# Performance work log

Hardware: AMD Instinct MI355X
Metric: run time of the kernel (lower is better)

Reference implementation:

```python
import jax, jax.numpy as jnp
import numpy as np

B, S, E, H, DH = 256, 256, 384, 6, 64
NEG_INF = -1e9


def setup_inputs() -> dict:
    key = jax.random.key(0)
    ks = jax.random.split(key, 8)
    sc = 0.02
    return {
        "x": jax.random.normal(ks[0], (B, S, E), jnp.float32),
        "Wq": jax.random.normal(ks[1], (H, E, DH), jnp.float32) * sc,
        "Wk": jax.random.normal(ks[2], (H, E, DH), jnp.float32) * sc,
        "Wv": jax.random.normal(ks[3], (H, E, DH), jnp.float32) * sc,
        "Wp": jax.random.normal(ks[4], (E, E), jnp.float32) * sc,
        "bp": jnp.zeros((E,), jnp.float32),
        "W1": jax.random.normal(ks[5], (E, 4 * E), jnp.float32) * sc,
        "b1": jnp.zeros((4 * E,), jnp.float32),
        "W2": jax.random.normal(ks[6], (4 * E, E), jnp.float32) * sc,
        "b2": jnp.zeros((E,), jnp.float32),
        "g1": jnp.ones((E,), jnp.float32),
        "be1": jnp.zeros((E,), jnp.float32),
        "g2": jnp.ones((E,), jnp.float32),
        "be2": jnp.zeros((E,), jnp.float32),
    }


def _layernorm(x, g, b, eps=1e-5):
    mu = jnp.mean(x, axis=-1, keepdims=True)
    var = jnp.mean(jnp.square(x - mu), axis=-1, keepdims=True)
    return (x - mu) * jax.lax.rsqrt(var + eps) * g + b


def reference(x, Wq, Wk, Wv, Wp, bp, W1, b1, W2, b2, g1, be1, g2, be2):
    # --- pre-attention LayerNorm ---
    h = _layernorm(x, g1, be1)
    # --- multi-head causal self-attention (all heads vectorized) ---
    q = jnp.einsum('bse,hed->bhsd', h, Wq)
    k = jnp.einsum('bse,hed->bhsd', h, Wk)
    v = jnp.einsum('bse,hed->bhsd', h, Wv)
    scores = jnp.einsum('bhsd,bhtd->bhst', q, k) * (DH ** -0.5)
    causal = jnp.tril(jnp.ones((S, S), dtype=bool))
    scores = jnp.where(causal, scores, NEG_INF)
    att = jax.nn.softmax(scores, axis=-1)  # dropout = identity at eval
    o = jnp.einsum('bhst,bhtd->bhsd', att, v)
    o = o.transpose(0, 2, 1, 3).reshape(x.shape[0], S, E)  # concat heads
    x = x + (o @ Wp + bp)
    # --- FFN block ---
    h2 = _layernorm(x, g2, be2)
    ffn = jax.nn.relu(h2 @ W1 + b1) @ W2 + b2
    return x + ffn
```

## Files before the change

### kernel.cpp

```cpp
#include <hip/hip_runtime.h>
#include <hip/hip_bf16.h>
#include <stdint.h>

typedef __bf16 bf16_t;
typedef __bf16 bf16x2 __attribute__((ext_vector_type(2)));
typedef __bf16 bf16x8 __attribute__((ext_vector_type(8)));
typedef float f32x4 __attribute__((ext_vector_type(4)));

#define NB 256
#define NS 256
#define NE 384
#define NH 6
#define ND 64
#define NM (NB*NS)

__device__ __forceinline__ f32x4 mfma16(bf16x8 a, bf16x8 b, f32x4 c) {
    return __builtin_amdgcn_mfma_f32_16x16x32_bf16(a, b, c, 0, 0, 0);
}

__device__ __forceinline__ void cp16_async(const bf16_t* g, const bf16_t* l) {
    __builtin_amdgcn_global_load_lds(
        (__attribute__((address_space(1))) void*)g,
        (__attribute__((address_space(3))) void*)l, 16, 0, 0);
}

__global__ void wqkv_trans(const float* __restrict__ Wq, const float* __restrict__ Wk,
                           const float* __restrict__ Wv, bf16_t* __restrict__ Wcat)
{
    int i = blockIdx.x * 256 + threadIdx.x;
    if (i >= NH*NE*ND) return;
    int d = i & 63;
    int e = (i >> 6) % NE;
    int h = i / (NE*ND);
    int n = h*64 + d;
    Wcat[(size_t)(0*NE*NH*ND) + (size_t)n*NE + e]            = (bf16_t)Wq[i];
    Wcat[(size_t)(NE)*(NH*ND) + (size_t)(384 + n)*NE + e - (size_t)(NE)*(NH*ND)] = (bf16_t)Wk[i];
    Wcat[(size_t)(768 + n)*NE + e]                            = (bf16_t)Wv[i];
}

__global__ void wtrans(const float* __restrict__ src, bf16_t* __restrict__ dst, int K, int N)
{
    int i = blockIdx.x * 256 + threadIdx.x;
    if (i >= K*N) return;
    int k = i / N, n = i % N;
    dst[(size_t)n*K + k] = (bf16_t)src[i];
}

__global__ __launch_bounds__(256) void ln_kernel(
    const float* __restrict__ x, const float* __restrict__ g,
    const float* __restrict__ be, bf16_t* __restrict__ o)
{
    const int wave = threadIdx.x >> 6, lane = threadIdx.x & 63;
    const int row = blockIdx.x * 4 + wave;
    const float* xr = x + (size_t)row * NE;
    float v[6]; float s = 0.f, sq = 0.f;
    #pragma unroll
    for (int i = 0; i < 6; i++) { v[i] = xr[i*64 + lane]; s += v[i]; sq += v[i]*v[i]; }
    #pragma unroll
    for (int off = 32; off > 0; off >>= 1) { s += __shfl_xor(s, off); sq += __shfl_xor(sq, off); }
    const float mean = s * (1.f/NE);
    const float rstd = rsqrtf(sq * (1.f/NE) - mean*mean + 1e-5f);
    bf16_t* orow = o + (size_t)row * NE;
    #pragma unroll
    for (int i = 0; i < 6; i++) {
        int e = i*64 + lane;
        orow[e] = (bf16_t)((v[i] - mean) * rstd * g[e] + be[e]);
    }
}

template<int OUT_MODE, bool RELU>
__global__ __launch_bounds__(256, 3) void gemm_bt(
    const bf16_t* __restrict__ A, const bf16_t* __restrict__ Bt,
    void* __restrict__ outp, const float* __restrict__ bias,
    const float* __restrict__ res, int M, int N, int K, int ldb)
{
    __shared__ bf16_t sA[3][128*32];
    __shared__ bf16_t sB[3][128*32];
    const int tid = threadIdx.x;
    const int wave = tid >> 6, lane = tid & 63;
    const int l15 = lane & 15, quad = lane >> 4;
    const int m0 = blockIdx.x * 128;
    const int n0 = blockIdx.y * 128;
    const int wm = wave >> 1, wn = wave & 1;

    const int srow = lane >> 2;
    const int scol = (lane & 3) * 8;
    const bf16_t* gA = A  + (size_t)(m0 + 32*wave + srow) * K + scol;
    const bf16_t* gB = Bt + (size_t)(n0 + 32*wave + srow) * ldb + scol;

    const f32x4 zero = {0.f, 0.f, 0.f, 0.f};
    f32x4 acc[4][4];
    #pragma unroll
    for (int a = 0; a < 4; a++)
        #pragma unroll
        for (int b = 0; b < 4; b++) acc[a][b] = zero;

    const int nk = K >> 5;

    auto issue = [&](int t, int slot) {
        const int kt = t << 5;
        cp16_async(gA + kt,                 &sA[slot][(32*wave)*32]);
        cp16_async(gA + (size_t)16*K + kt,  &sA[slot][(32*wave + 16)*32]);
        cp16_async(gB + kt,                 &sB[slot][(32*wave)*32]);
        cp16_async(gB + (size_t)16*ldb + kt,&sB[slot][(32*wave + 16)*32]);
    };

    issue(0, 0);
    issue(1, 1);

    int cb = 0;
    int ns = 2;
    for (int it = 0; it < nk; ++it) {
        asm volatile("s_barrier" ::: "memory");
        if (it + 2 < nk) {
            issue(it + 2, ns);
            asm volatile("s_waitcnt vmcnt(8)\n\ts_barrier" ::: "memory");
        } else if (it + 1 < nk) {
            asm volatile("s_waitcnt vmcnt(4)\n\ts_barrier" ::: "memory");
        } else {
            asm volatile("s_waitcnt vmcnt(0)\n\ts_barrier" ::: "memory");
        }

        bf16x8 af[4], bfr[4];
        #pragma unroll
        for (int i = 0; i < 4; i++)
            af[i] = *(const bf16x8*)&sA[cb][(64*wm + 16*i + l15)*32 + quad*8];
        #pragma unroll
        for (int i = 0; i < 4; i++)
            bfr[i] = *(const bf16x8*)&sB[cb][(64*wn + 16*i + l15)*32 + quad*8];
        #pragma unroll
        for (int mi = 0; mi < 4; mi++)
            #pragma unroll
            for (int ni = 0; ni < 4; ni++)
                acc[mi][ni] = mfma16(af[mi], bfr[ni], acc[mi][ni]);

        cb = (cb == 2) ? 0 : cb + 1;
        ns = (ns == 2) ? 0 : ns + 1;
    }

    #pragma unroll
    for (int mi = 0; mi < 4; mi++) {
        #pragma unroll
        for (int ni = 0; ni < 4; ni++) {
            #pragma unroll
            for (int r = 0; r < 4; r++) {
                int gm = m0 + 64*wm + 16*mi + quad*4 + r;
                int gn = n0 + 64*wn + 16*ni + l15;
                float v = acc[mi][ni][r];
                if (bias) v += bias[gn];
                if (res)  v += res[(size_t)gm*N + gn];
                if (RELU) v = fmaxf(v, 0.f);
                if (OUT_MODE == 1) {
                    int sel = (gn >= 768) ? 2 : ((gn >= 384) ? 1 : 0);
                    int within = gn - sel*384;
                    int b = gm >> 8, s = gm & 255, h = within >> 6, d = within & 63;
                    ((bf16_t*)outp)[(size_t)sel*((size_t)NM*384) +
                                    (((size_t)b*NH + h)*NS + s)*ND + d] = (bf16_t)v;
                } else if (OUT_MODE == 2) {
                    ((float*)outp)[(size_t)gm*N + gn] = v;
                } else {
                    ((bf16_t*)outp)[(size_t)gm*N + gn] = (bf16_t)v;
                }
            }
        }
    }
}

__global__ __launch_bounds__(256) void attn_kernel(
    const bf16_t* __restrict__ Qg, const bf16_t* __restrict__ Kg,
    const bf16_t* __restrict__ Vg, bf16_t* __restrict__ Og)
{
    __shared__ bf16_t sK[256*72];
    __shared__ bf16_t sVT[64*264];
    __shared__ bf16_t sQ[64*72];
    __shared__ bf16_t sS[64*264];
    __shared__ float sMax[64*4];
    __shared__ float sSum[64*4];
    __shared__ float sRowSum[64];

    const int tid = threadIdx.x;
    const int wave = tid >> 6, lane = tid & 63;
    const int l15 = lane & 15, quad = lane >> 4;
    const int bh = blockIdx.x;
    const int b = bh / NH, h = bh % NH;
    const size_t base = (size_t)bh * (NS*ND);
    const bf16_t* Qb = Qg + base;
    const bf16_t* Kb = Kg + base;
    const bf16_t* Vb = Vg + base;

    #pragma unroll
    for (int it = 0; it < 8; it++) {
        int idx = it*256 + tid;
        int t = idx >> 3, c = idx & 7;
        bf16x8 kv = *(const bf16x8*)(Kb + t*64 + c*8);
        *(bf16x8*)&sK[t*72 + c*8] = kv;
        bf16x8 vv = *(const bf16x8*)(Vb + t*64 + c*8);
        #pragma unroll
        for (int j = 0; j < 8; j++) sVT[(c*8 + j)*264 + t] = vv[j];
    }

    const int r = lane;
    const int p = wave;
    const f32x4 zero = {0.f, 0.f, 0.f, 0.f};

    for (int mt = 0; mt < 4; mt++) {
        __syncthreads();
        #pragma unroll
        for (int it = 0; it < 2; it++) {
            int idx = it*256 + tid;
            int qr = idx >> 3, c = idx & 7;
            *(bf16x8*)&sQ[qr*72 + c*8] = *(const bf16x8*)(Qb + (64*mt + qr)*64 + c*8);
        }
        __syncthreads();
        if (wave <= mt) {
            const int ct = wave;
            bf16x8 bk[2][4];
            #pragma unroll
            for (int ks = 0; ks < 2; ks++)
                #pragma unroll
                for (int ni = 0; ni < 4; ni++)
                    bk[ks][ni] = *(const bf16x8*)&sK[(64*ct + 16*ni + l15)*72 + ks*32 + quad*8];
            #pragma unroll
            for (int mi = 0; mi < 4; mi++) {
                bf16x8 a0 = *(const bf16x8*)&sQ[(16*mi + l15)*72 + quad*8];
                bf16x8 a1 = *(const bf16x8*)&sQ[(16*mi + l15)*72 + 32 + quad*8];
                f32x4 sc[4];
                #pragma unroll
                for (int ni = 0; ni < 4; ni++) sc[ni] = zero;
                #pragma unroll
                for (int ni = 0; ni < 4; ni++) sc[ni] = mfma16(a0, bk[0][ni], sc[ni]);
                #pragma unroll
                for (int ni = 0; ni < 4; ni++) sc[ni] = mfma16(a1, bk[1][ni], sc[ni]);
                #pragma unroll
                for (int ni = 0; ni < 4; ni++)
                    #pragma unroll
                    for (int rr = 0; rr < 4; rr++)
                        sS[(16*mi + quad*4 + rr)*264 + 64*ct + 16*ni + l15] =
                            (bf16_t)(sc[ni][rr] * 0.125f);
            }
        }
        __syncthreads();
        const int sg = 64*mt + r;
        float mx = -INFINITY;
        if (p <= mt) {
            #pragma unroll
            for (int c = 0; c < 8; c++) {
                bf16x8 v8 = *(const bf16x8*)&sS[r*264 + 64*p + c*8];
                #pragma unroll
                for (int j = 0; j < 8; j++) {
                    int t = 64*p + c*8 + j;
                    float v = (float)v8[j];
                    mx = (t <= sg) ? fmaxf(mx, v) : mx;
                }
            }
        }
        sMax[r*4 + p] = mx;
        __syncthreads();
        const float rmax = fmaxf(fmaxf(sMax[r*4+0], sMax[r*4+1]),
                                 fmaxf(sMax[r*4+2], sMax[r*4+3]));
        float sum = 0.f;
        if (p <= mt) {
            #pragma unroll
            for (int c = 0; c < 8; c++) {
                bf16x8 v8 = *(const bf16x8*)&sS[r*264 + 64*p + c*8];
                bf16x8 e8;
                #pragma unroll
                for (int j = 0; j < 8; j++) {
                    int t = 64*p + c*8 + j;
                    float e = 0.f;
                    if (t <= sg) e = __expf((float)v8[j] - rmax);
                    sum += e;
                    e8[j] = (bf16_t)e;
                }
                *(bf16x8*)&sS[r*264 + 64*p + c*8] = e8;
            }
        }
        sSum[r*4 + p] = sum;
        __syncthreads();
        if (p == 0) sRowSum[r] = sSum[r*4+0] + sSum[r*4+1] + sSum[r*4+2] + sSum[r*4+3];
        __syncthreads();
        f32x4 oacc[4];
        #pragma unroll
        for (int ni = 0; ni < 4; ni++) oacc[ni] = zero;
        for (int kt = 0; kt <= mt; kt++) {
            bf16x8 a = *(const bf16x8*)&sS[(16*p + l15)*264 + 64*kt + quad*8];
            #pragma unroll
            for (int ni = 0; ni < 4; ni++) {
                bf16x8 bv = *(const bf16x8*)&sVT[(16*ni + l15)*264 + 64*kt + quad*8];
                oacc[ni] = mfma16(a, bv, oacc[ni]);
            }
        }
        #pragma unroll
        for (int ni = 0; ni < 4; ni++) {
            #pragma unroll
            for (int rr = 0; rr < 4; rr++) {
                int lrow = 16*p + quad*4 + rr;
                float inv = 1.0f / sRowSum[lrow];
                int srow_g = 64*mt + lrow;
                int d = 16*ni + l15;
                Og[((size_t)(b*NS + srow_g))*NE + h*ND + d] = (bf16_t)(oacc[ni][rr] * inv);
            }
        }
    }
}

extern "C" void kernel_launch(void* const* d_in, const int* in_sizes, int n_in,
                              void* d_out, int out_size, void* d_ws, size_t ws_size,
                              hipStream_t stream)
{
    (void)in_sizes; (void)n_in; (void)out_size; (void)ws_size;
    const float* x   = (const float*)d_in[0];
    const float* Wq  = (const float*)d_in[1];
    const float* Wk  = (const float*)d_in[2];
    const float* Wv  = (const float*)d_in[3];
    const float* Wp  = (const float*)d_in[4];
    const float* bp  = (const float*)d_in[5];
    const float* W1  = (const float*)d_in[6];
    const float* b1  = (const float*)d_in[7];
    const float* W2  = (const float*)d_in[8];
    const float* b2  = (const float*)d_in[9];
    const float* g1  = (const float*)d_in[10];
    const float* be1 = (const float*)d_in[11];
    const float* g2  = (const float*)d_in[12];
    const float* be2 = (const float*)d_in[13];
    float* out = (float*)d_out;

    char* ws = (char*)d_ws;
    const size_t SZ = (size_t)NM * NE * 2;
    bf16_t* h_bf  = (bf16_t*)(ws);
    bf16_t* q_bf  = (bf16_t*)(ws + SZ);
    bf16_t* k_bf  = (bf16_t*)(ws + 2*SZ);
    bf16_t* v_bf  = (bf16_t*)(ws + 3*SZ);
    bf16_t* o_bf  = (bf16_t*)(ws);
    bf16_t* h2_bf = (bf16_t*)(ws);
    bf16_t* hid   = (bf16_t*)(ws + SZ);
    char* wb = ws + 4*SZ;
    bf16_t* Wcat = (bf16_t*)(wb);
    bf16_t* Wpt  = (bf16_t*)(wb + 884736);
    bf16_t* W1t  = (bf16_t*)(wb + 884736 + 294912);
    bf16_t* W2t  = (bf16_t*)(wb + 884736 + 294912 + 1179648);

    wqkv_trans<<<(NH*NE*ND + 255)/256, 256, 0, stream>>>(Wq, Wk, Wv, Wcat);
    wtrans<<<(NE*NE + 255)/256, 256, 0, stream>>>(Wp, Wpt, NE, NE);
    wtrans<<<(NE*4*NE + 255)/256, 256, 0, stream>>>(W1, W1t, NE, 4*NE);
    wtrans<<<(NE*4*NE + 255)/256, 256, 0, stream>>>(W2, W2t, 4*NE, NE);

    ln_kernel<<<NM/4, 256, 0, stream>>>(x, g1, be1, h_bf);

    dim3 gqkv(NM/128, 9), g384(NM/128, 3), gffn(NM/128, 6);
    gemm_bt<1,false><<<gqkv, 256, 0, stream>>>(h_bf, Wcat, q_bf, nullptr, nullptr, NM, 1152, NE, NE);

    attn_kernel<<<NB*NH, 256, 0, stream>>>(q_bf, k_bf, v_bf, o_bf);

    gemm_bt<2,false><<<g384, 256, 0, stream>>>(o_bf, Wpt, out, bp, x, NM, NE, NE, NE);

    ln_kernel<<<NM/4, 256, 0, stream>>>(out, g2, be2, h2_bf);

    gemm_bt<3,true ><<<gffn, 256, 0, stream>>>(h2_bf, W1t, hid, b1, nullptr, NM, 768, NE, NE);
    gemm_bt<2,false><<<g384, 256, 0, stream>>>(hid, W2t, out, b2, out, NM, NE, 768, 1536);

    gemm_bt<3,true ><<<gffn, 256, 0, stream>>>(h2_bf, W1t + (size_t)768*NE, hid, b1 + 768, nullptr, NM, 768, NE, NE);
    gemm_bt<2,false><<<g384, 256, 0, stream>>>(hid, W2t + 768, out, nullptr, out, NM, NE, 768, 1536);
}
```

Measured before the change: 1.015 ms.

## Widen GEMM tiles to 128x384 with 512-thread blocks and a shared LDS buffer

Replaces the 128x128 GEMM kernel with one that computes a 128x384 output tile using 8 waves. Each wave produces a 64x96 sub-tile (4x6 MFMA accumulators), and A and B share a single triple-buffered LDS array. Two waves load A and six load B. The wider tile means each A row tile is fetched from global memory once per 384 output columns, cutting redundant A reads for the N=384/768/1152 GEMMs. In exchange it uses more registers and LDS per block (96KB LDS), which lowers occupancy, and the grid has fewer blocks.

```diff
diff --git a/kernel.cpp b/kernel.cpp
--- a/kernel.cpp
+++ b/kernel.cpp
@@ -69,40 +69,42 @@
 }
 
 template<int OUT_MODE, bool RELU>
-__global__ __launch_bounds__(256, 3) void gemm_bt(
+__global__ __launch_bounds__(512, 2) void gemm_wide(
     const bf16_t* __restrict__ A, const bf16_t* __restrict__ Bt,
     void* __restrict__ outp, const float* __restrict__ bias,
     const float* __restrict__ res, int M, int N, int K, int ldb)
 {
-    __shared__ bf16_t sA[3][128*32];
-    __shared__ bf16_t sB[3][128*32];
+    __shared__ bf16_t sAB[3][512*32];
     const int tid = threadIdx.x;
     const int wave = tid >> 6, lane = tid & 63;
     const int l15 = lane & 15, quad = lane >> 4;
     const int m0 = blockIdx.x * 128;
-    const int n0 = blockIdx.y * 128;
-    const int wm = wave >> 1, wn = wave & 1;
+    const int n0 = blockIdx.y * 384;
+    const int wm = wave >> 2, wn = wave & 3;
 
     const int srow = lane >> 2;
     const int scol = (lane & 3) * 8;
-    const bf16_t* gA = A  + (size_t)(m0 + 32*wave + srow) * K + scol;
-    const bf16_t* gB = Bt + (size_t)(n0 + 32*wave + srow) * ldb + scol;
+    const int r0 = 64 * wave;
+
+    const bf16_t* gsrc;
+    size_t rs;
+    if (wave < 2) { gsrc = A  + (size_t)(m0 + r0 + srow) * K + scol;              rs = (size_t)K; }
+    else          { gsrc = Bt + (size_t)(n0 + r0 - 128 + srow) * ldb + scol;      rs = (size_t)ldb; }
 
     const f32x4 zero = {0.f, 0.f, 0.f, 0.f};
-    f32x4 acc[4][4];
+    f32x4 acc[4][6];
     #pragma unroll
     for (int a = 0; a < 4; a++)
         #pragma unroll
-        for (int b = 0; b < 4; b++) acc[a][b] = zero;
+        for (int b = 0; b < 6; b++) acc[a][b] = zero;
 
     const int nk = K >> 5;
 
     auto issue = [&](int t, int slot) {
         const int kt = t << 5;
-        cp16_async(gA + kt,                 &sA[slot][(32*wave)*32]);
-        cp16_async(gA + (size_t)16*K + kt,  &sA[slot][(32*wave + 16)*32]);
-        cp16_async(gB + kt,                 &sB[slot][(32*wave)*32]);
-        cp16_async(gB + (size_t)16*ldb + kt,&sB[slot][(32*wave + 16)*32]);
+        #pragma unroll
+        for (int i = 0; i < 4; i++)
+            cp16_async(gsrc + (size_t)(16*i)*rs + kt, &sAB[slot][(r0 + 16*i)*32]);
     };
 
     issue(0, 0);
@@ -121,18 +123,17 @@
             asm volatile("s_waitcnt vmcnt(0)\n\ts_barrier" ::: "memory");
         }
 
-        bf16x8 af[4], bfr[4];
-        #pragma unroll
-        for (int i = 0; i < 4; i++)
-            af[i] = *(const bf16x8*)&sA[cb][(64*wm + 16*i + l15)*32 + quad*8];
-        #pragma unroll
-        for (int i = 0; i < 4; i++)
-            bfr[i] = *(const bf16x8*)&sB[cb][(64*wn + 16*i + l15)*32 + quad*8];
-        #pragma unroll
-        for (int mi = 0; mi < 4; mi++)
-            #pragma unroll
-            for (int ni = 0; ni < 4; ni++)
-                acc[mi][ni] = mfma16(af[mi], bfr[ni], acc[mi][ni]);
+        bf16x8 bfr[6];
+        #pragma unroll
+        for (int i = 0; i < 6; i++)
+            bfr[i] = *(const bf16x8*)&sAB[cb][(128 + 96*wn + 16*i + l15)*32 + quad*8];
+        #pragma unroll
+        for (int mi = 0; mi < 4; mi++) {
+            bf16x8 af = *(const bf16x8*)&sAB[cb][(64*wm + 16*mi + l15)*32 + quad*8];
+            #pragma unroll
+            for (int ni = 0; ni < 6; ni++)
+                acc[mi][ni] = mfma16(af, bfr[ni], acc[mi][ni]);
+        }
 
         cb = (cb == 2) ? 0 : cb + 1;
         ns = (ns == 2) ? 0 : ns + 1;
@@ -141,11 +142,11 @@
     #pragma unroll
     for (int mi = 0; mi < 4; mi++) {
         #pragma unroll
-        for (int ni = 0; ni < 4; ni++) {
+        for (int ni = 0; ni < 6; ni++) {
             #pragma unroll
             for (int r = 0; r < 4; r++) {
                 int gm = m0 + 64*wm + 16*mi + quad*4 + r;
-                int gn = n0 + 64*wn + 16*ni + l15;
+                int gn = n0 + 96*wn + 16*ni + l15;
                 float v = acc[mi][ni][r];
                 if (bias) v += bias[gn];
                 if (res)  v += res[(size_t)gm*N + gn];
@@ -347,18 +348,18 @@
 
     ln_kernel<<<NM/4, 256, 0, stream>>>(x, g1, be1, h_bf);
 
-    dim3 gqkv(NM/128, 9), g384(NM/128, 3), gffn(NM/128, 6);
-    gemm_bt<1,false><<<gqkv, 256, 0, stream>>>(h_bf, Wcat, q_bf, nullptr, nullptr, NM, 1152, NE, NE);
+    dim3 gqkv(NM/128, 3), g1col(NM/128, 1), g2col(NM/128, 2);
+    gemm_wide<1,false><<<gqkv, 512, 0, stream>>>(h_bf, Wcat, q_bf, nullptr, nullptr, NM, 1152, NE, NE);
 
     attn_kernel<<<NB*NH, 256, 0, stream>>>(q_bf, k_bf, v_bf, o_bf);
 
-    gemm_bt<2,false><<<g384, 256, 0, stream>>>(o_bf, Wpt, out, bp, x, NM, NE, NE, NE);
+    gemm_wide<2,false><<<g1col, 512, 0, stream>>>(o_bf, Wpt, out, bp, x, NM, NE, NE, NE);
 
     ln_kernel<<<NM/4, 256, 0, stream>>>(out, g2, be2, h2_bf);
 
-    gemm_bt<3,true ><<<gffn, 256, 0, stream>>>(h2_bf, W1t, hid, b1, nullptr, NM, 768, NE, NE);
-    gemm_bt<2,false><<<g384, 256, 0, stream>>>(hid, W2t, out, b2, out, NM, NE, 768, 1536);
-
-    gemm_bt<3,true ><<<gffn, 256, 0, stream>>>(h2_bf, W1t + (size_t)768*NE, hid, b1 + 768, nullptr, NM, 768, NE, NE);
-    gemm_bt<2,false><<<g384, 256, 0, stream>>>(hid, W2t + 768, out, nullptr, out, NM, NE, 768, 1536);
-}
+    gemm_wide<3,true ><<<g2col, 512, 0, stream>>>(h2_bf, W1t, hid, b1, nullptr, NM, 768, NE, NE);
+    gemm_wide<2,false><<<g1col, 512, 0, stream>>>(hid, W2t, out, b2, out, NM, NE, 768, 1536);
+
+    gemm_wide<3,true ><<<g2col, 512, 0, stream>>>(h2_bf, W1t + (size_t)768*NE, hid, b1 + 768, nullptr, NM, 768, NE, NE);
+    gemm_wide<2,false><<<g1col, 512, 0, stream>>>(hid, W2t + 768, out, nullptr, out, NM, NE, 768, 1536);
+}
```

Result: slower. 1.061 ms (+4.6%).
